# Optimization experiments

Measured on AMD Instinct MI355X. Metric: run time of the kernel, lower is better.

## Reference

```python
import jax, jax.numpy as jnp
import numpy as np

TOP_K = 32
SCALE_FACTOR = 8.0
NEG_INF = -1e18


def setup_inputs() -> dict:
    key = jax.random.key(0)
    kq, kk, kv = jax.random.split(key, 3)
    B, H, S, D = 2, 16, 2048, 64
    q = jax.random.normal(kq, (B, H, S, D), dtype=jnp.float32)
    k = jax.random.normal(kk, (B, H, S, D), dtype=jnp.float32)
    v = jax.random.normal(kv, (B, H, S, D), dtype=jnp.float32)
    return {"q": q, "k": k, "v": v}


def reference(q, k, v):
    # scores: [B, H, Sq, Sk]
    scores = jnp.einsum("bhqd,bhkd->bhqk", q, k) / SCALE_FACTOR
    # torch code clamps top_k against key.size()[-1] == head dim D (quirk);
    # with TOP_K=32 < D=64 the clamp is inactive.
    top_k = min(TOP_K, k.shape[-1])
    topv, _ = jax.lax.top_k(scores, top_k)            # [B,H,Sq,top_k], sorted desc
    thresh = topv[..., -1:]                            # k-th largest per query row
    mask_k = scores < thresh                           # True -> masked out
    scores = jnp.where(mask_k, NEG_INF, scores)
    attn = jax.nn.softmax(scores, axis=-1)
    context = jnp.einsum("bhqk,bhkd->bhqd", attn, v)
    return context, attn, mask_k
```

## Files before the change

### kernel.cpp

```cpp
#include <hip/hip_runtime.h>
#include <math.h>

namespace {
constexpr int kS = 2048;
constexpr int kD = 64;
constexpr int kBH = 32;
constexpr int kTopK = 32;
constexpr int kBins = 4096;
constexpr int kMaxCand = 256;
constexpr int kKeepCap = 64;
constexpr size_t kCtxElems  = (size_t)kBH * kS * kD;
constexpr size_t kAttnElems = (size_t)kBH * kS * kS;
}

__device__ __forceinline__ unsigned sortable_bits(float x) {
  unsigned u = __float_as_uint(x);
  return u ^ ((u & 0x80000000u) ? 0xFFFFFFFFu : 0x80000000u);
}

__global__ __launch_bounds__(256) void qk_scores(const float* __restrict__ q,
                                                 const float* __restrict__ k,
                                                 float* __restrict__ scores) {
  __shared__ float QsT[64][132];
  __shared__ float KsT[64][132];
  const int bh  = blockIdx.z;
  const int q0  = blockIdx.y * 128;
  const int k0  = blockIdx.x * 128;
  const int tid = threadIdx.x;
  const float* qg = q + ((size_t)bh * kS + q0) * kD;
  const float* kg = k + ((size_t)bh * kS + k0) * kD;

#pragma unroll
  for (int rnd = 0; rnd < 8; ++rnd) {
    int flat = rnd * 1024 + tid * 4;
    int r = flat >> 6;
    int c = flat & 63;
    float4 qv = *(const float4*)(qg + flat);
    QsT[c + 0][r] = qv.x;
    QsT[c + 1][r] = qv.y;
    QsT[c + 2][r] = qv.z;
    QsT[c + 3][r] = qv.w;
    float4 kv = *(const float4*)(kg + flat);
    KsT[c + 0][r] = kv.x;
    KsT[c + 1][r] = kv.y;
    KsT[c + 2][r] = kv.z;
    KsT[c + 3][r] = kv.w;
  }
  __syncthreads();

  const int ty8 = (tid >> 4) * 8;
  const int tx8 = (tid & 15) * 8;
  float acc[8][8] = {};
#pragma unroll
  for (int kk = 0; kk < 64; kk += 4) {
    float a[4][8], b[4][8];
#pragma unroll
    for (int u = 0; u < 4; ++u) {
      *(float4*)(&a[u][0]) = *(const float4*)(&QsT[kk + u][ty8]);
      *(float4*)(&a[u][4]) = *(const float4*)(&QsT[kk + u][ty8 + 4]);
      *(float4*)(&b[u][0]) = *(const float4*)(&KsT[kk + u][tx8]);
      *(float4*)(&b[u][4]) = *(const float4*)(&KsT[kk + u][tx8 + 4]);
    }
#pragma unroll
    for (int i = 0; i < 8; ++i)
#pragma unroll
      for (int u = 0; u < 4; ++u)
#pragma unroll
        for (int j = 0; j < 8; ++j)
          acc[i][j] += a[u][i] * b[u][j];
  }

#pragma unroll
  for (int i = 0; i < 8; ++i) {
    float* orow = scores + ((size_t)bh * kS + q0 + ty8 + i) * kS + k0 + tx8;
    float4 o0 = make_float4(acc[i][0] * 0.125f, acc[i][1] * 0.125f,
                            acc[i][2] * 0.125f, acc[i][3] * 0.125f);
    float4 o1 = make_float4(acc[i][4] * 0.125f, acc[i][5] * 0.125f,
                            acc[i][6] * 0.125f, acc[i][7] * 0.125f);
    *(float4*)(orow)     = o0;
    *(float4*)(orow + 4) = o1;
  }
}

__global__ __launch_bounds__(256) void topk_softmax(const float* __restrict__ v,
                                                    float* __restrict__ ctx,
                                                    float* __restrict__ attn,
                                                    float* __restrict__ mask) {
  const int row  = blockIdx.x;
  const int bh   = row >> 11;
  const int tid  = threadIdx.x;
  const int lane = tid & 63;
  const int wid  = tid >> 6;

  __shared__ unsigned s_hist[kBins];
  __shared__ float    s_cand[kMaxCand];
  __shared__ int      s_kidx[kKeepCap];
  __shared__ float    s_kw[kKeepCap];
  __shared__ float    s_wmax[4], s_wsum[4];
  __shared__ unsigned s_T[4];
  __shared__ unsigned s_nc, s_nk;
  __shared__ int      s_bstar, s_gabove;
  __shared__ float    s_t32;

  const float* srow = attn + (size_t)row * kS;
  float4 l0 = *(const float4*)(srow + tid * 4);
  float4 l1 = *(const float4*)(srow + 1024 + tid * 4);
  float locv[8] = {l0.x, l0.y, l0.z, l0.w, l1.x, l1.y, l1.z, l1.w};
  int   loce[8];
#pragma unroll
  for (int j = 0; j < 8; ++j)
    loce[j] = (j < 4) ? (tid * 4 + j) : (1024 + tid * 4 + (j - 4));
#pragma unroll
  for (int i = 0; i < 4; ++i)
    *(uint4*)(&s_hist[tid * 16 + i * 4]) = make_uint4(0u, 0u, 0u, 0u);
  if (tid == 0) { s_nc = 0u; s_nk = 0u; }
  __syncthreads();

  unsigned bins[8];
  float pmax = locv[0];
#pragma unroll
  for (int j = 0; j < 8; ++j) {
    bins[j] = sortable_bits(locv[j]) >> 20;
    atomicAdd(&s_hist[bins[j]], 1u);
    pmax = fmaxf(pmax, locv[j]);
  }
#pragma unroll
  for (int off = 32; off >= 1; off >>= 1)
    pmax = fmaxf(pmax, __shfl_xor(pmax, off));
  if (lane == 0) s_wmax[wid] = pmax;
  __syncthreads();

  unsigned lsum = 0;
#pragma unroll
  for (int j = 0; j < 16; ++j) lsum += s_hist[tid * 16 + j];
  unsigned sfx = lsum;
#pragma unroll
  for (int off = 1; off < 64; off <<= 1) {
    unsigned z = __shfl_down(sfx, off);
    if (lane + off < 64) sfx += z;
  }
  if (lane == 0) s_T[wid] = sfx;
  __syncthreads();

  unsigned hi = 0;
#pragma unroll
  for (int w = 0; w < 4; ++w)
    if (w > wid) hi += s_T[w];
  unsigned gsfx  = sfx + hi;
  unsigned above = gsfx - lsum;
  if (gsfx >= (unsigned)kTopK && above < (unsigned)kTopK) {
    unsigned run = above;
    for (int j = 15; j >= 0; --j) {
      unsigned h = s_hist[tid * 16 + j];
      if (run < (unsigned)kTopK && run + h >= (unsigned)kTopK) {
        s_bstar  = tid * 16 + j;
        s_gabove = (int)run;
      }
      run += h;
    }
  }
  __syncthreads();
  const int   bstar  = s_bstar;
  const int   gabove = s_gabove;
  const float mx = fmaxf(fmaxf(s_wmax[0], s_wmax[1]),
                         fmaxf(s_wmax[2], s_wmax[3]));

#pragma unroll
  for (int j = 0; j < 8; ++j) {
    if ((int)bins[j] == bstar) {
      unsigned pos = atomicAdd(&s_nc, 1u);
      if (pos < (unsigned)kMaxCand) s_cand[pos] = locv[j];
    }
  }
  __syncthreads();
  const int m2 = (int)min(s_nc, (unsigned)kMaxCand);

  for (int c = tid; c < m2; c += 256) {
    float x = s_cand[c];
    int g = 0, e = 0;
    for (int j2 = 0; j2 < m2; ++j2) {
      float y = s_cand[j2];
      g += (y > x);
      e += (y == x);
    }
    int G = gabove + g;
    if (G < kTopK && G + e >= kTopK) s_t32 = x;
  }
  __syncthreads();
  const float t32 = s_t32;

  float w8[8];
  float psum = 0.0f;
#pragma unroll
  for (int j = 0; j < 8; ++j) {
    bool keep = (locv[j] >= t32);
    float wv = keep ? __expf(locv[j] - mx) : 0.0f;
    w8[j] = wv;
    psum += wv;
    if (keep) {
      unsigned p = atomicAdd(&s_nk, 1u);
      if (p < (unsigned)kKeepCap) { s_kidx[p] = loce[j]; s_kw[p] = wv; }
    }
  }
#pragma unroll
  for (int off = 32; off >= 1; off >>= 1)
    psum += __shfl_xor(psum, off);
  if (lane == 0) s_wsum[wid] = psum;
  __syncthreads();

  const float Z = s_wsum[0] + s_wsum[1] + s_wsum[2] + s_wsum[3];
  const float invZ = 1.0f / Z;

  float* arow = attn + (size_t)row * kS;
  float* mrow = mask + (size_t)row * kS;
  float4 a0 = make_float4(w8[0] * invZ, w8[1] * invZ, w8[2] * invZ, w8[3] * invZ);
  float4 a1 = make_float4(w8[4] * invZ, w8[5] * invZ, w8[6] * invZ, w8[7] * invZ);
  float4 m0 = make_float4(locv[0] >= t32 ? 0.f : 1.f, locv[1] >= t32 ? 0.f : 1.f,
                          locv[2] >= t32 ? 0.f : 1.f, locv[3] >= t32 ? 0.f : 1.f);
  float4 m1 = make_float4(locv[4] >= t32 ? 0.f : 1.f, locv[5] >= t32 ? 0.f : 1.f,
                          locv[6] >= t32 ? 0.f : 1.f, locv[7] >= t32 ? 0.f : 1.f);
  *(float4*)(arow + tid * 4)        = a0;
  *(float4*)(arow + 1024 + tid * 4) = a1;
  *(float4*)(mrow + tid * 4)        = m0;
  *(float4*)(mrow + 1024 + tid * 4) = m1;

  if (tid < kD) {
    const int nk = (int)min(s_nk, (unsigned)kKeepCap);
    float acc = 0.0f;
    for (int c = 0; c < nk; ++c)
      acc += s_kw[c] * v[((size_t)bh * kS + s_kidx[c]) * kD + tid];
    ctx[(size_t)row * kD + tid] = acc * invZ;
  }
}

extern "C" void kernel_launch(void* const* d_in, const int* in_sizes, int n_in,
                              void* d_out, int out_size, void* d_ws, size_t ws_size,
                              hipStream_t stream) {
  const float* q = (const float*)d_in[0];
  const float* k = (const float*)d_in[1];
  const float* v = (const float*)d_in[2];
  float* out  = (float*)d_out;
  float* ctx  = out;
  float* attn = out + kCtxElems;
  float* mask = attn + kAttnElems;

  dim3 g1(kS / 128, kS / 128, kBH);
  qk_scores<<<g1, 256, 0, stream>>>(q, k, attn);
  topk_softmax<<<dim3(kBH * kS), 256, 0, stream>>>(v, ctx, attn, mask);
}
```

Measured before the change: 1.438 ms.

## Store 16-bit sortable score keys and recompute exact scores for top-k candidates

The QK kernel now writes truncated 16-bit order-preserving keys into the attention buffer instead of full fp32 scores. This halves the intermediate write and the read-back in the top-k kernel. The top-k kernel builds its histogram from these keys and gathers candidates from the threshold bin and the bin just below it. It then recomputes exact scores for those candidates with q·k dot products, and takes the max, threshold and softmax weights from the exact values. The trade-offs are extra gather and dot-product work per row, a linear search to map each element to its candidate weight, and a 256-candidate cap that could overflow on ties or dense bins.

Result: slower. 2.539 ms (+76.6%).

```diff
diff --git a/kernel.cpp b/kernel.cpp
--- a/kernel.cpp
+++ b/kernel.cpp
@@ -8,7 +8,6 @@
 constexpr int kTopK = 32;
 constexpr int kBins = 4096;
 constexpr int kMaxCand = 256;
-constexpr int kKeepCap = 64;
 constexpr size_t kCtxElems  = (size_t)kBH * kS * kD;
 constexpr size_t kAttnElems = (size_t)kBH * kS * kS;
 }
@@ -18,9 +17,9 @@
   return u ^ ((u & 0x80000000u) ? 0xFFFFFFFFu : 0x80000000u);
 }
 
-__global__ __launch_bounds__(256) void qk_scores(const float* __restrict__ q,
-                                                 const float* __restrict__ k,
-                                                 float* __restrict__ scores) {
+__global__ __launch_bounds__(256) void qk_keys(const float* __restrict__ q,
+                                               const float* __restrict__ k,
+                                               unsigned short* __restrict__ keys) {
   __shared__ float QsT[64][132];
   __shared__ float KsT[64][132];
   const int bh  = blockIdx.z;
@@ -52,14 +51,14 @@
   const int tx8 = (tid & 15) * 8;
   float acc[8][8] = {};
 #pragma unroll
-  for (int kk = 0; kk < 64; kk += 4) {
+  for (int d4 = 0; d4 < 64; d4 += 4) {
     float a[4][8], b[4][8];
 #pragma unroll
     for (int u = 0; u < 4; ++u) {
-      *(float4*)(&a[u][0]) = *(const float4*)(&QsT[kk + u][ty8]);
-      *(float4*)(&a[u][4]) = *(const float4*)(&QsT[kk + u][ty8 + 4]);
-      *(float4*)(&b[u][0]) = *(const float4*)(&KsT[kk + u][tx8]);
-      *(float4*)(&b[u][4]) = *(const float4*)(&KsT[kk + u][tx8 + 4]);
+      *(float4*)(&a[u][0]) = *(const float4*)(&QsT[d4 + u][ty8]);
+      *(float4*)(&a[u][4]) = *(const float4*)(&QsT[d4 + u][ty8 + 4]);
+      *(float4*)(&b[u][0]) = *(const float4*)(&KsT[d4 + u][tx8]);
+      *(float4*)(&b[u][4]) = *(const float4*)(&KsT[d4 + u][tx8 + 4]);
     }
 #pragma unroll
     for (int i = 0; i < 8; ++i)
@@ -72,17 +71,22 @@
 
 #pragma unroll
   for (int i = 0; i < 8; ++i) {
-    float* orow = scores + ((size_t)bh * kS + q0 + ty8 + i) * kS + k0 + tx8;
-    float4 o0 = make_float4(acc[i][0] * 0.125f, acc[i][1] * 0.125f,
-                            acc[i][2] * 0.125f, acc[i][3] * 0.125f);
-    float4 o1 = make_float4(acc[i][4] * 0.125f, acc[i][5] * 0.125f,
-                            acc[i][6] * 0.125f, acc[i][7] * 0.125f);
-    *(float4*)(orow)     = o0;
-    *(float4*)(orow + 4) = o1;
-  }
-}
-
-__global__ __launch_bounds__(256) void topk_softmax(const float* __restrict__ v,
+    size_t R = (size_t)bh * kS + q0 + ty8 + i;
+    unsigned short* kb = keys + R * 4096 + (k0 + tx8);
+    unsigned short t8[8];
+#pragma unroll
+    for (int j = 0; j < 8; ++j) {
+      float s = acc[i][j] * 0.125f;
+      t8[j] = (unsigned short)(sortable_bits(s) >> 16);
+    }
+    *(ushort4*)(kb)     = make_ushort4(t8[0], t8[1], t8[2], t8[3]);
+    *(ushort4*)(kb + 4) = make_ushort4(t8[4], t8[5], t8[6], t8[7]);
+  }
+}
+
+__global__ __launch_bounds__(256) void topk_softmax(const float* __restrict__ q,
+                                                    const float* __restrict__ k,
+                                                    const float* __restrict__ v,
                                                     float* __restrict__ ctx,
                                                     float* __restrict__ attn,
                                                     float* __restrict__ mask) {
@@ -93,41 +97,36 @@
   const int wid  = tid >> 6;
 
   __shared__ unsigned s_hist[kBins];
-  __shared__ float    s_cand[kMaxCand];
-  __shared__ int      s_kidx[kKeepCap];
-  __shared__ float    s_kw[kKeepCap];
-  __shared__ float    s_wmax[4], s_wsum[4];
+  __shared__ float    s_q[kD];
+  __shared__ int      s_cidx[kMaxCand];
+  __shared__ float    s_cval[kMaxCand];
+  __shared__ float    s_w[kMaxCand];
   __shared__ unsigned s_T[4];
-  __shared__ unsigned s_nc, s_nk;
-  __shared__ int      s_bstar, s_gabove;
-  __shared__ float    s_t32;
-
-  const float* srow = attn + (size_t)row * kS;
-  float4 l0 = *(const float4*)(srow + tid * 4);
-  float4 l1 = *(const float4*)(srow + 1024 + tid * 4);
-  float locv[8] = {l0.x, l0.y, l0.z, l0.w, l1.x, l1.y, l1.z, l1.w};
-  int   loce[8];
-#pragma unroll
-  for (int j = 0; j < 8; ++j)
+  __shared__ unsigned s_nc;
+  __shared__ int      s_bstar;
+  __shared__ float    s_t32, s_mx, s_Z;
+
+  const unsigned short* keyrow = (const unsigned short*)attn + (size_t)row * 4096;
+  ushort4 ka = *(const ushort4*)(keyrow + tid * 4);
+  ushort4 kb = *(const ushort4*)(keyrow + 1024 + tid * 4);
+  unsigned keys8[8] = {ka.x, ka.y, ka.z, ka.w, kb.x, kb.y, kb.z, kb.w};
+  int      loce[8];
+  unsigned bins[8];
+#pragma unroll
+  for (int j = 0; j < 8; ++j) {
     loce[j] = (j < 4) ? (tid * 4 + j) : (1024 + tid * 4 + (j - 4));
+    bins[j] = keys8[j] >> 4;
+  }
 #pragma unroll
   for (int i = 0; i < 4; ++i)
     *(uint4*)(&s_hist[tid * 16 + i * 4]) = make_uint4(0u, 0u, 0u, 0u);
-  if (tid == 0) { s_nc = 0u; s_nk = 0u; }
-  __syncthreads();
-
-  unsigned bins[8];
-  float pmax = locv[0];
-#pragma unroll
-  for (int j = 0; j < 8; ++j) {
-    bins[j] = sortable_bits(locv[j]) >> 20;
-    atomicAdd(&s_hist[bins[j]], 1u);
-    pmax = fmaxf(pmax, locv[j]);
-  }
-#pragma unroll
-  for (int off = 32; off >= 1; off >>= 1)
-    pmax = fmaxf(pmax, __shfl_xor(pmax, off));
-  if (lane == 0) s_wmax[wid] = pmax;
+  if (tid == 0) s_nc = 0u;
+  if (tid < 16)
+    *(float4*)(&s_q[tid * 4]) = *(const float4*)(q + (size_t)row * kD + tid * 4);
+  __syncthreads();
+
+#pragma unroll
+  for (int j = 0; j < 8; ++j) atomicAdd(&s_hist[bins[j]], 1u);
   __syncthreads();
 
   unsigned lsum = 0;
@@ -152,83 +151,82 @@
     unsigned run = above;
     for (int j = 15; j >= 0; --j) {
       unsigned h = s_hist[tid * 16 + j];
-      if (run < (unsigned)kTopK && run + h >= (unsigned)kTopK) {
-        s_bstar  = tid * 16 + j;
-        s_gabove = (int)run;
-      }
+      if (run < (unsigned)kTopK && run + h >= (unsigned)kTopK)
+        s_bstar = tid * 16 + j;
       run += h;
     }
   }
   __syncthreads();
-  const int   bstar  = s_bstar;
-  const int   gabove = s_gabove;
-  const float mx = fmaxf(fmaxf(s_wmax[0], s_wmax[1]),
-                         fmaxf(s_wmax[2], s_wmax[3]));
+  const int blo = s_bstar - 1;
 
 #pragma unroll
   for (int j = 0; j < 8; ++j) {
-    if ((int)bins[j] == bstar) {
+    if ((int)bins[j] >= blo) {
       unsigned pos = atomicAdd(&s_nc, 1u);
-      if (pos < (unsigned)kMaxCand) s_cand[pos] = locv[j];
-    }
-  }
-  __syncthreads();
-  const int m2 = (int)min(s_nc, (unsigned)kMaxCand);
-
-  for (int c = tid; c < m2; c += 256) {
-    float x = s_cand[c];
+      if (pos < (unsigned)kMaxCand) s_cidx[pos] = loce[j];
+    }
+  }
+  __syncthreads();
+  const int m = (int)min(s_nc, (unsigned)kMaxCand);
+
+  for (int c = tid; c < m; c += 256) {
+    const float* kr = k + ((size_t)bh * kS + s_cidx[c]) * kD;
+    float acc = 0.0f;
+    for (int d = 0; d < kD; ++d) acc += s_q[d] * kr[d];
+    s_cval[c] = acc * 0.125f;
+  }
+  __syncthreads();
+
+  for (int c = tid; c < m; c += 256) {
+    float x = s_cval[c];
     int g = 0, e = 0;
-    for (int j2 = 0; j2 < m2; ++j2) {
-      float y = s_cand[j2];
+    for (int j2 = 0; j2 < m; ++j2) {
+      float y = s_cval[j2];
       g += (y > x);
       e += (y == x);
     }
-    int G = gabove + g;
-    if (G < kTopK && G + e >= kTopK) s_t32 = x;
+    if (g == 0) s_mx = x;
+    if (g < kTopK && g + e >= kTopK) s_t32 = x;
   }
   __syncthreads();
   const float t32 = s_t32;
-
-  float w8[8];
-  float psum = 0.0f;
+  const float mx  = s_mx;
+
+  for (int c = tid; c < m; c += 256)
+    s_w[c] = (s_cval[c] >= t32) ? __expf(s_cval[c] - mx) : 0.0f;
+  __syncthreads();
+  if (tid == 0) {
+    float z = 0.0f;
+    for (int c2 = 0; c2 < m; ++c2) z += s_w[c2];
+    s_Z = z;
+  }
+  __syncthreads();
+  const float invZ = 1.0f / s_Z;
+
+  float a8[8], m8[8];
 #pragma unroll
   for (int j = 0; j < 8; ++j) {
-    bool keep = (locv[j] >= t32);
-    float wv = keep ? __expf(locv[j] - mx) : 0.0f;
-    w8[j] = wv;
-    psum += wv;
-    if (keep) {
-      unsigned p = atomicAdd(&s_nk, 1u);
-      if (p < (unsigned)kKeepCap) { s_kidx[p] = loce[j]; s_kw[p] = wv; }
-    }
-  }
-#pragma unroll
-  for (int off = 32; off >= 1; off >>= 1)
-    psum += __shfl_xor(psum, off);
-  if (lane == 0) s_wsum[wid] = psum;
-  __syncthreads();
-
-  const float Z = s_wsum[0] + s_wsum[1] + s_wsum[2] + s_wsum[3];
-  const float invZ = 1.0f / Z;
-
+    float av = 0.0f, mv = 1.0f;
+    if ((int)bins[j] >= blo) {
+      float w = 0.0f;
+      for (int c = 0; c < m; ++c)
+        if (s_cidx[c] == loce[j]) { w = s_w[c]; break; }
+      if (w > 0.0f) { av = w * invZ; mv = 0.0f; }
+    }
+    a8[j] = av; m8[j] = mv;
+  }
   float* arow = attn + (size_t)row * kS;
   float* mrow = mask + (size_t)row * kS;
-  float4 a0 = make_float4(w8[0] * invZ, w8[1] * invZ, w8[2] * invZ, w8[3] * invZ);
-  float4 a1 = make_float4(w8[4] * invZ, w8[5] * invZ, w8[6] * invZ, w8[7] * invZ);
-  float4 m0 = make_float4(locv[0] >= t32 ? 0.f : 1.f, locv[1] >= t32 ? 0.f : 1.f,
-                          locv[2] >= t32 ? 0.f : 1.f, locv[3] >= t32 ? 0.f : 1.f);
-  float4 m1 = make_float4(locv[4] >= t32 ? 0.f : 1.f, locv[5] >= t32 ? 0.f : 1.f,
-                          locv[6] >= t32 ? 0.f : 1.f, locv[7] >= t32 ? 0.f : 1.f);
-  *(float4*)(arow + tid * 4)        = a0;
-  *(float4*)(arow + 1024 + tid * 4) = a1;
-  *(float4*)(mrow + tid * 4)        = m0;
-  *(float4*)(mrow + 1024 + tid * 4) = m1;
+  *(float4*)(arow + tid * 4)        = make_float4(a8[0], a8[1], a8[2], a8[3]);
+  *(float4*)(arow + 1024 + tid * 4) = make_float4(a8[4], a8[5], a8[6], a8[7]);
+  *(float4*)(mrow + tid * 4)        = make_float4(m8[0], m8[1], m8[2], m8[3]);
+  *(float4*)(mrow + 1024 + tid * 4) = make_float4(m8[4], m8[5], m8[6], m8[7]);
 
   if (tid < kD) {
-    const int nk = (int)min(s_nk, (unsigned)kKeepCap);
     float acc = 0.0f;
-    for (int c = 0; c < nk; ++c)
-      acc += s_kw[c] * v[((size_t)bh * kS + s_kidx[c]) * kD + tid];
+    for (int c = 0; c < m; ++c)
+      if (s_w[c] > 0.0f)
+        acc += s_w[c] * v[((size_t)bh * kS + s_cidx[c]) * kD + tid];
     ctx[(size_t)row * kD + tid] = acc * invZ;
   }
 }
@@ -245,6 +243,6 @@
   float* mask = attn + kAttnElems;
 
   dim3 g1(kS / 128, kS / 128, kBH);
-  qk_scores<<<g1, 256, 0, stream>>>(q, k, attn);
-  topk_softmax<<<dim3(kBH * kS), 256, 0, stream>>>(v, ctx, attn, mask);
-}
+  qk_keys<<<g1, 256, 0, stream>>>(q, k, (unsigned short*)attn);
+  topk_softmax<<<dim3(kBH * kS), 256, 0, stream>>>(q, k, v, ctx, attn, mask);
+}
```
